# Kernel tuning notes

Hardware: AMD Instinct MI355X
Metric: run time of the kernel (lower is better)

## Reference

```python
import jax, jax.numpy as jnp
import numpy as np


def setup_inputs() -> dict:
    key = jax.random.key(0)
    ks = jax.random.split(key, 11)
    B, n, d_x, d = 8, 2048, 128, 512
    H, hd = 8, 64  # num_heads, head_size = d_v // num_heads
    std_key = d ** -0.5      # d_k ** -0.5 (d_k = 512 after mlp rep)
    std_val = d ** -0.5      # d_v ** -0.5
    return {
        "x1": jax.random.normal(ks[0], (B, n, d_x), jnp.float32),
        "x2": jax.random.normal(ks[1], (B, n, d_x), jnp.float32),
        "r": jax.random.normal(ks[2], (B, n, d), jnp.float32),
        # BatchLinear (shared mlp rep): d_x -> 512 -> 512
        "W1": jax.random.normal(ks[3], (d_x, d), jnp.float32) * (d_x ** -0.5),
        "b1": jnp.zeros((d,), jnp.float32),
        "W2": jax.random.normal(ks[4], (d, d), jnp.float32) * (d ** -0.5),
        "b2": jnp.zeros((d,), jnp.float32),
        # per-head 1x1-conv projections, stacked over heads: [H, out, in]
        "Wq": jax.random.normal(ks[5], (H, hd, d), jnp.float32) * std_key,
        "Wk": jax.random.normal(ks[6], (H, hd, d), jnp.float32) * std_key,
        "Wv": jax.random.normal(ks[7], (H, hd, d), jnp.float32) * std_key,
        "Wo": jax.random.normal(ks[8], (H, d, hd), jnp.float32) * std_val,
    }


def reference(x1, x2, r, W1, b1, W2, b2, Wq, Wk, Wv, Wo):
    # rep == 'mlp': shared BatchLinear applied to x1 (keys) and x2 (queries)
    def mlp(x):  # [B,n,d_x] -> [B,n,512]; relu on all but last layer
        h = jax.nn.relu(jnp.einsum("bnd,de->bne", x, W1) + b1)
        return jnp.einsum("bnd,de->bne", h, W2) + b2

    k = mlp(x1)  # [B,n1,d_k]
    q = mlp(x2)  # [B,n2,d_k]

    # multihead: per-head 1x1 convs == linear projections; batched over heads
    qh = jnp.einsum("bmd,hed->bhme", q, Wq)  # [B,H,m,hd]
    kh = jnp.einsum("bnd,hed->bhne", k, Wk)  # [B,H,n,hd]
    vh = jnp.einsum("bnd,hed->bhne", r, Wv)  # [B,H,n,hd]

    scale = jnp.sqrt(jnp.asarray(qh.shape[-1], qh.dtype))
    scores = jnp.einsum("bhme,bhne->bhmn", qh, kh) / scale
    w = jax.nn.softmax(scores, axis=-1)      # normalise=True
    o = jnp.einsum("bhmn,bhne->bhme", w, vh)  # [B,H,m,hd]

    # per-head output conv (hd -> d_v), summed over heads
    rep = jnp.einsum("bhme,hde->bmd", o, Wo)  # [B,m,d_v]
    return rep
```

## Files before the change

### kernel.cpp

```cpp
#include <hip/hip_runtime.h>
#include <stdint.h>

typedef __attribute__((ext_vector_type(8))) short short8;
typedef __attribute__((ext_vector_type(4))) float f32x4;
typedef __attribute__((ext_vector_type(16))) float f32x16;
typedef __attribute__((ext_vector_type(4))) unsigned u32x4;

#define DEVINL __device__ __forceinline__

DEVINL unsigned short f2bf(float f) {
  unsigned u = __float_as_uint(f);
  u = (u + 0x7FFFu + ((u >> 16) & 1u)) >> 16;
  return (unsigned short)u;
}

DEVINL void gload_lds16(const void* g, void* lds) {
  __builtin_amdgcn_global_load_lds(
      (const __attribute__((address_space(1))) unsigned int*)g,
      (__attribute__((address_space(3))) unsigned int*)lds, 16, 0, 0);
}

DEVINL float fexp2(float x) {
  float r;
  asm("v_exp_f32 %0, %1" : "=v"(r) : "v"(x));
  return r;
}

DEVINL unsigned cvtpk(float lo, float hi) {
  unsigned r;
  asm("v_cvt_pk_bf16_f32 %0, %1, %2" : "=v"(r) : "v"(lo), "v"(hi));
  return r;
}

DEVINL void pl32swap(unsigned& a, unsigned& b) {
  asm("v_permlane32_swap_b32 %0, %1" : "+v"(a), "+v"(b));
}


__global__ void cvt_wquad(const float* __restrict__ W2, const float* __restrict__ Wq,
                          const float* __restrict__ Wk, const float* __restrict__ Wv,
                          unsigned short* __restrict__ W2B, unsigned short* __restrict__ WqB,
                          unsigned short* __restrict__ WkB, unsigned short* __restrict__ WvB) {
  const int a = blockIdx.x >> 8;
  const int i = (blockIdx.x & 255) * 256 + threadIdx.x;
  const float* src = (a == 0) ? W2 : (a == 1) ? Wq : (a == 2) ? Wk : Wv;
  unsigned short* dst = (a == 0) ? W2B : (a == 1) ? WqB : (a == 2) ? WkB : WvB;
  const float scale = (a == 1) ? 0.18033688f : 1.0f;
  float4 v = ((const float4*)src)[i];
  ushort4 o;
  o.x = f2bf(v.x * scale); o.y = f2bf(v.y * scale);
  o.z = f2bf(v.z * scale); o.w = f2bf(v.w * scale);
  ((ushort4*)dst)[i] = o;
}

__global__ void prep_misc(const float* __restrict__ W1, const float* __restrict__ Wo,
                          const float* __restrict__ b2, const float* __restrict__ Wq,
                          const float* __restrict__ Wk,
                          unsigned short* __restrict__ W1T, unsigned short* __restrict__ WoT,
                          float* __restrict__ bqf, float* __restrict__ bkf) {
  const int bid = blockIdx.x, tid = threadIdx.x;
  if (bid < 256) {
    int idx = bid * 256 + tid;
    int n = idx >> 7, k = idx & 127;
    W1T[idx] = f2bf(W1[(size_t)k * 512 + n]);
  } else if (bid < 1280) {
    int idx = (bid - 256) * 256 + tid;
    int d = idx >> 9, j = idx & 511, h = j >> 6, e = j & 63;
    WoT[idx] = f2bf(Wo[(size_t)h * 32768 + (size_t)d * 64 + e]);
  } else {
    int rid = (bid - 1280) * 4 + (tid >> 6);
    int l = tid & 63;
    int e = rid & 511, which = rid >> 9;
    const float* W = which ? Wk : Wq;
    float scale = which ? 1.0f : 0.18033688f;
    float acc = 0.f;
#pragma unroll
    for (int j = 0; j < 8; ++j)
      acc += b2[l * 8 + j] * W[(size_t)e * 512 + l * 8 + j];
    acc *= scale;
#pragma unroll
    for (int off = 1; off < 64; off <<= 1) acc += __shfl_xor(acc, off, 64);
    if (l == 0) (which ? bkf : bqf)[e] = acc;
  }
}

__global__ void cvt_all(const float* __restrict__ x1, const float* __restrict__ x2,
                        const float* __restrict__ r,
                        unsigned short* __restrict__ Xb, unsigned short* __restrict__ Rb) {
  const int bid = blockIdx.x, tid = threadIdx.x;
  const float* src;
  unsigned short* dst;
  int i;
  if (bid < 2048)      { src = x1; dst = Xb;           i = bid * 256 + tid; }
  else if (bid < 4096) { src = x2; dst = Xb + 2097152; i = (bid - 2048) * 256 + tid; }
  else                 { src = r;  dst = Rb;           i = (bid - 4096) * 256 + tid; }
  float4 v = ((const float4*)src)[i];
  ushort4 o;
  o.x = f2bf(v.x); o.y = f2bf(v.y); o.z = f2bf(v.z); o.w = f2bf(v.w);
  ((ushort4*)dst)[i] = o;
}

__global__ __launch_bounds__(256) void v_transpose(const unsigned short* __restrict__ VH,
                                                   unsigned short* __restrict__ VT) {
  const int bh = blockIdx.x, t = blockIdx.y;
  const int b = bh >> 3, h = bh & 7;
  __shared__ __align__(16) unsigned short L[128 * 72];
  const int tid = threadIdx.x;
#pragma unroll
  for (int i = 0; i < 4; ++i) {
    int c = i * 256 + tid, kk = c >> 3, cr = c & 7;
    *(short8*)&L[kk * 72 + cr * 8] =
        *(const short8*)&VH[(size_t)(b * 2048 + t * 128 + kk) * 512 + h * 64 + cr * 8];
  }
  __syncthreads();
#pragma unroll
  for (int i = 0; i < 4; ++i) {
    int c = i * 256 + tid, e = c >> 4, ckn = c & 15;
    short8 v;
#pragma unroll
    for (int j = 0; j < 8; ++j) v[j] = L[(ckn * 8 + j) * 72 + e];
    *(short8*)&VT[((size_t)bh * 64 + e) * 2048 + t * 128 + ckn * 8] = v;
  }
}

template <bool RELU, typename TOut>
__global__ __launch_bounds__(256) void gemm64(
    const unsigned short* A0, const unsigned short* B0, const float* bias0, TOut* C0,
    const unsigned short* A1, const unsigned short* B1, const float* bias1, TOut* C1,
    const unsigned short* A2, const unsigned short* B2, const float* bias2, TOut* C2,
    int M, int N, int K) {
  __shared__ __align__(16) char smem[32768];
  unsigned short* As = (unsigned short*)smem;
  unsigned short* Bs = (unsigned short*)(smem + 16384);

  const int z = blockIdx.z;
  const unsigned short* A = (z == 0) ? A0 : (z == 1) ? A1 : A2;
  const unsigned short* Bt = (z == 0) ? B0 : (z == 1) ? B1 : B2;
  const float* bias = (z == 0) ? bias0 : (z == 1) ? bias1 : bias2;
  TOut* C = (z == 0) ? C0 : (z == 1) ? C1 : C2;

  const int nx = gridDim.x;
  int id = blockIdx.y * nx + blockIdx.x;
  const int nwg = nx * gridDim.y;
  if ((nwg & 7) == 0) id = (id & 7) * (nwg >> 3) + (id >> 3);
  const int n0 = (id % nx) * 128, m0 = (id / nx) * 128;

  const int tid = threadIdx.x, w = tid >> 6, l = tid & 63;
  const int wm = w >> 1, wn = w & 1;
  const int lr = l & 15, lg = l >> 4;

  f32x4 zero4 = {0.f, 0.f, 0.f, 0.f};
  f32x4 acc[4][4];
#pragma unroll
  for (int i = 0; i < 4; ++i)
#pragma unroll
    for (int j = 0; j < 4; ++j) acc[i][j] = zero4;

  for (int k0 = 0; k0 < K; k0 += 64) {
#pragma unroll
    for (int i = 0; i < 4; ++i) {
      const int c = i * 256 + tid;
      const int row = c >> 3, ch = c & 7;
      const int sl = (ch ^ (row & 7)) * 8;
      gload_lds16(A + (size_t)(m0 + row) * K + k0 + sl, (char*)As + c * 16);
      gload_lds16(Bt + (size_t)(n0 + row) * K + k0 + sl, (char*)Bs + c * 16);
    }
    asm volatile("s_waitcnt vmcnt(0)" ::: "memory");
    __syncthreads();

#pragma unroll
    for (int kk = 0; kk < 2; ++kk) {
      short8 af[4], bfr[4];
#pragma unroll
      for (int mi = 0; mi < 4; ++mi) {
        const int row = wm * 64 + mi * 16 + lr;
        af[mi] = *(const short8*)((const char*)As + row * 128 + (((kk * 4 + lg) ^ (row & 7)) * 16));
      }
#pragma unroll
      for (int ni = 0; ni < 4; ++ni) {
        const int row = wn * 64 + ni * 16 + lr;
        bfr[ni] = *(const short8*)((const char*)Bs + row * 128 + (((kk * 4 + lg) ^ (row & 7)) * 16));
      }
#pragma unroll
      for (int mi = 0; mi < 4; ++mi)
#pragma unroll
        for (int ni = 0; ni < 4; ++ni)
          acc[mi][ni] = __builtin_amdgcn_mfma_f32_16x16x32_bf16(af[mi], bfr[ni], acc[mi][ni], 0, 0, 0);
    }
    __syncthreads();
  }

#pragma unroll
  for (int ni = 0; ni < 4; ++ni) {
    const int col = n0 + wn * 64 + ni * 16 + lr;
    const float bv = bias ? bias[col] : 0.f;
#pragma unroll
    for (int mi = 0; mi < 4; ++mi) {
      const int row = m0 + wm * 64 + mi * 16 + lg * 4;
#pragma unroll
      for (int r = 0; r < 4; ++r) {
        float v = acc[mi][ni][r] + bv;
        if (RELU) v = fmaxf(v, 0.f);
        if constexpr (sizeof(TOut) == 2)
          C[(size_t)(row + r) * N + col] = (TOut)f2bf(v);
        else
          C[(size_t)(row + r) * N + col] = v;
      }
    }
  }
}

DEVINL void stage_kv(const unsigned short* Kp, const unsigned short* Vp,
                     char* kb, char* vb, int tid, int k0) {
  const int row = tid >> 3, cs = tid & 7;
  const int sl = (cs ^ (row & 7)) * 8;
  gload_lds16(Kp + (size_t)(k0 + row) * 512 + sl, kb + tid * 16);
  gload_lds16(Vp + (size_t)row * 2048 + k0 + sl, vb + tid * 16);
}

__global__ __launch_bounds__(512) void attn_sw(
    const unsigned short* __restrict__ Q, const unsigned short* __restrict__ Kh,
    const unsigned short* __restrict__ VT, unsigned short* __restrict__ O) {
  const int bh = blockIdx.x, b = bh >> 3, h = bh & 7;
  const int q0 = blockIdx.y * 256;
  const int tid = threadIdx.x, w = tid >> 6, l = tid & 63;
  const int lq = l & 31, hi = l >> 5;
  const size_t baseBH = (size_t)b * 2048 * 512 + (size_t)h * 64;

  __shared__ __align__(16) char smem[49152];
  char* vb0 = smem + 24576;

  const unsigned short* Kp = Kh + baseBH;
  const unsigned short* Vp = VT + (size_t)bh * 64 * 2048;

  short8 qf[4];
  {
    const unsigned short* qp = Q + baseBH + (size_t)(q0 + w * 32 + lq) * 512 + hi * 8;
#pragma unroll
    for (int kc = 0; kc < 4; ++kc) qf[kc] = *(const short8*)(qp + kc * 16);
  }

  f32x16 ot0 = {0,0,0,0,0,0,0,0,0,0,0,0,0,0,0,0};
  f32x16 ot1 = {0,0,0,0,0,0,0,0,0,0,0,0,0,0,0,0};
  float m_run = -1e30f, l_run = 0.f;
  const int xs = (lq & 7);

  stage_kv(Kp, Vp, smem, vb0, tid, 0);
  stage_kv(Kp, Vp, smem + 8192, vb0 + 8192, tid, 64);

  for (int t = 0; t < 32; ++t) {
    if (t < 31) asm volatile("s_waitcnt vmcnt(2)" ::: "memory");
    else        asm volatile("s_waitcnt vmcnt(0)" ::: "memory");
    __syncthreads();
    if (t < 30) {
      const int tn = t + 2, rb = tn - (tn / 3) * 3;
      stage_kv(Kp, Vp, smem + rb * 8192, vb0 + rb * 8192, tid, tn * 64);
    }
    const int cb = t - (t / 3) * 3;
    const char* klc = smem + cb * 8192;
    const char* vtc = vb0 + cb * 8192;

    f32x16 st0 = {0,0,0,0,0,0,0,0,0,0,0,0,0,0,0,0};
    f32x16 st1 = {0,0,0,0,0,0,0,0,0,0,0,0,0,0,0,0};
    __builtin_amdgcn_s_setprio(1);
#pragma unroll
    for (int kc = 0; kc < 4; ++kc) {
      const int sl = ((kc * 2 + hi) ^ xs) * 16;
      short8 kf0 = *(const short8*)(klc + lq * 128 + sl);
      short8 kf1 = *(const short8*)(klc + (32 + lq) * 128 + sl);
      st0 = __builtin_amdgcn_mfma_f32_32x32x16_bf16(kf0, qf[kc], st0, 0, 0, 0);
      st1 = __builtin_amdgcn_mfma_f32_32x32x16_bf16(kf1, qf[kc], st1, 0, 0, 0);
    }
    __builtin_amdgcn_s_setprio(0);

    float t8[8];
#pragma unroll
    for (int r = 0; r < 8; ++r)
      t8[r] = fmaxf(fmaxf(st0[r], st0[r + 8]), fmaxf(st1[r], st1[r + 8]));
    float mt = fmaxf(fmaxf(fmaxf(t8[0], t8[1]), fmaxf(t8[2], t8[3])),
                     fmaxf(fmaxf(t8[4], t8[5]), fmaxf(t8[6], t8[7])));
    mt = fmaxf(mt, __shfl_xor(mt, 32, 64));

    if (__any(mt > m_run + 8.0f)) {
      float mn = fmaxf(m_run, mt);
      float al = fexp2(m_run - mn);
      m_run = mn;
      l_run *= al;
#pragma unroll
      for (int r = 0; r < 16; ++r) { ot0[r] *= al; ot1[r] *= al; }
    }
#pragma unroll
    for (int r = 0; r < 16; ++r) {
      st0[r] = fexp2(st0[r] - m_run);
      st1[r] = fexp2(st1[r] - m_run);
    }
    float s8[8];
#pragma unroll
    for (int r = 0; r < 8; ++r)
      s8[r] = (st0[r] + st0[r + 8]) + (st1[r] + st1[r + 8]);
    float rs = ((s8[0] + s8[1]) + (s8[2] + s8[3])) + ((s8[4] + s8[5]) + (s8[6] + s8[7]));
    rs += __shfl_xor(rs, 32, 64);
    l_run += rs;

    __builtin_amdgcn_s_setprio(1);
#pragma unroll
    for (int kc = 0; kc < 4; ++kc) {
      const int c = kc & 1;
      float p0, p1, p2, p3, p4, p5, p6, p7;
      if (kc < 2) {
        p0 = st0[8*c+0]; p1 = st0[8*c+1]; p2 = st0[8*c+2]; p3 = st0[8*c+3];
        p4 = st0[8*c+4]; p5 = st0[8*c+5]; p6 = st0[8*c+6]; p7 = st0[8*c+7];
      } else {
        p0 = st1[8*c+0]; p1 = st1[8*c+1]; p2 = st1[8*c+2]; p3 = st1[8*c+3];
        p4 = st1[8*c+4]; p5 = st1[8*c+5]; p6 = st1[8*c+6]; p7 = st1[8*c+7];
      }
      unsigned X0 = cvtpk(p0, p1), X1 = cvtpk(p2, p3);
      unsigned Y0 = cvtpk(p4, p5), Y1 = cvtpk(p6, p7);
      pl32swap(X0, Y0);
      pl32swap(X1, Y1);
      u32x4 u = {X0, X1, Y0, Y1};
      short8 pfk = __builtin_bit_cast(short8, u);

      const int sl = ((kc * 2 + hi) ^ xs) * 16;
      short8 v0 = *(const short8*)(vtc + lq * 128 + sl);
      short8 v1 = *(const short8*)(vtc + (32 + lq) * 128 + sl);
      ot0 = __builtin_amdgcn_mfma_f32_32x32x16_bf16(v0, pfk, ot0, 0, 0, 0);
      ot1 = __builtin_amdgcn_mfma_f32_32x32x16_bf16(v1, pfk, ot1, 0, 0, 0);
    }
    __builtin_amdgcn_s_setprio(0);
  }

  __syncthreads();

  unsigned short (*eps)[32][66] = (unsigned short (*)[32][66])smem;
  const float rinv = 1.0f / l_run;
#pragma unroll
  for (int r = 0; r < 16; ++r) {
    const int e = (r & 3) + 8 * (r >> 2) + 4 * hi;
    eps[w][lq][e] = f2bf(ot0[r] * rinv);
    eps[w][lq][e + 32] = f2bf(ot1[r] * rinv);
  }
  asm volatile("s_waitcnt lgkmcnt(0)" ::: "memory");
  __builtin_amdgcn_sched_barrier(0);
#pragma unroll
  for (int i = 0; i < 4; ++i) {
    const int qq = i * 8 + (l >> 3), e0 = (l & 7) * 8;
    short8 v = *(const short8*)&eps[w][qq][e0];
    *(short8*)(O + baseBH + (size_t)(q0 + w * 32 + qq) * 512 + e0) = v;
  }
}


extern "C" void kernel_launch(void* const* d_in, const int* in_sizes, int n_in,
                              void* d_out, int out_size, void* d_ws, size_t ws_size,
                              hipStream_t stream) {
  const float* x1 = (const float*)d_in[0];
  const float* x2 = (const float*)d_in[1];
  const float* r  = (const float*)d_in[2];
  const float* W1 = (const float*)d_in[3];
  const float* b1 = (const float*)d_in[4];
  const float* W2 = (const float*)d_in[5];
  const float* b2 = (const float*)d_in[6];
  const float* Wq = (const float*)d_in[7];
  const float* Wk = (const float*)d_in[8];
  const float* Wv = (const float*)d_in[9];
  const float* Wo = (const float*)d_in[10];

  char* ws = (char*)d_ws;
  size_t off = 0;
  auto alloc = [&](size_t bytes) {
    char* p = ws + off;
    off = (off + bytes + 255) & ~(size_t)255;
    return p;
  };
  unsigned short* W1T = (unsigned short*)alloc(512 * 128 * 2);
  unsigned short* W2B = (unsigned short*)alloc(512 * 512 * 2);
  unsigned short* WqB = (unsigned short*)alloc(512 * 512 * 2);
  unsigned short* WkB = (unsigned short*)alloc(512 * 512 * 2);
  unsigned short* WvB = (unsigned short*)alloc(512 * 512 * 2);
  unsigned short* WoT = (unsigned short*)alloc(512 * 512 * 2);
  unsigned short* Fq  = (unsigned short*)alloc(512 * 512 * 2);
  unsigned short* Fk  = (unsigned short*)alloc(512 * 512 * 2);
  float* bqf = (float*)alloc(512 * 4);
  float* bkf = (float*)alloc(512 * 4);
  unsigned short* Xb  = (unsigned short*)alloc((size_t)32768 * 128 * 2);
  unsigned short* Hb  = (unsigned short*)alloc((size_t)32768 * 512 * 2);
  unsigned short* Rb  = (unsigned short*)alloc((size_t)16384 * 512 * 2);
  unsigned short* QHb = (unsigned short*)alloc((size_t)16384 * 512 * 2);
  unsigned short* KHb = (unsigned short*)alloc((size_t)16384 * 512 * 2);
  unsigned short* VHb = (unsigned short*)alloc((size_t)16384 * 512 * 2);
  unsigned short* VT  = Rb;
  unsigned short* Ob  = QHb;

  cvt_wquad<<<1024, 256, 0, stream>>>(W2, Wq, Wk, Wv, W2B, WqB, WkB, WvB);
  prep_misc<<<1536, 256, 0, stream>>>(W1, Wo, b2, Wq, Wk, W1T, WoT, bqf, bkf);
  gemm64<false, unsigned short><<<dim3(4, 4, 2), 256, 0, stream>>>(
      WqB, W2B, nullptr, Fq,  WkB, W2B, nullptr, Fk,  WkB, W2B, nullptr, Fk,
      512, 512, 512);
  cvt_all<<<12288, 256, 0, stream>>>(x1, x2, r, Xb, Rb);
  gemm64<true, unsigned short><<<dim3(4, 256, 1), 256, 0, stream>>>(
      Xb, W1T, b1, Hb,  Xb, W1T, b1, Hb,  Xb, W1T, b1, Hb,
      32768, 512, 128);
  gemm64<false, unsigned short><<<dim3(4, 128, 3), 256, 0, stream>>>(
      Hb, Fk, bkf, KHb,
      Hb + (size_t)16384 * 512, Fq, bqf, QHb,
      Rb, WvB, nullptr, VHb,
      16384, 512, 512);
  v_transpose<<<dim3(64, 16), 256, 0, stream>>>(VHb, VT);
  attn_sw<<<dim3(64, 8), 512, 0, stream>>>(QHb, KHb, VT, Ob);
  gemm64<false, float><<<dim3(4, 128, 1), 256, 0, stream>>>(
      Ob, WoT, nullptr, (float*)d_out,  Ob, WoT, nullptr, (float*)d_out,
      Ob, WoT, nullptr, (float*)d_out,
      16384, 512, 512);
}
```

Measured before the change: 200.3 us.

## Process two query blocks per wave in attention to reuse K/V fragments

Each wave now handles 64 query rows (two 32-row blocks) instead of 32, so every K and V fragment read from LDS serves two sets of MFMAs, and the grid shrinks from 512 to 256 blocks. K and V fragments are loaded once into registers per tile, and __syncthreads is replaced with a bare s_barrier. The goal is less LDS traffic and fewer global K/V reloads per query, at the cost of more registers per thread and half as many blocks, which may hurt occupancy or load balance on a GPU with many CUs.

```diff
diff --git a/kernel.cpp b/kernel.cpp
--- a/kernel.cpp
+++ b/kernel.cpp
@@ -218,135 +218,165 @@
   gload_lds16(Vp + (size_t)row * 2048 + k0 + sl, vb + tid * 16);
 }
 
-__global__ __launch_bounds__(512) void attn_sw(
+__global__ __launch_bounds__(512, 2) void attn_sw2(
     const unsigned short* __restrict__ Q, const unsigned short* __restrict__ Kh,
     const unsigned short* __restrict__ VT, unsigned short* __restrict__ O) {
   const int bh = blockIdx.x, b = bh >> 3, h = bh & 7;
-  const int q0 = blockIdx.y * 256;
+  const int q0 = blockIdx.y * 512;
   const int tid = threadIdx.x, w = tid >> 6, l = tid & 63;
   const int lq = l & 31, hi = l >> 5;
   const size_t baseBH = (size_t)b * 2048 * 512 + (size_t)h * 64;
 
   __shared__ __align__(16) char smem[49152];
-  char* vb0 = smem + 24576;
 
   const unsigned short* Kp = Kh + baseBH;
   const unsigned short* Vp = VT + (size_t)bh * 64 * 2048;
 
-  short8 qf[4];
-  {
-    const unsigned short* qp = Q + baseBH + (size_t)(q0 + w * 32 + lq) * 512 + hi * 8;
-#pragma unroll
-    for (int kc = 0; kc < 4; ++kc) qf[kc] = *(const short8*)(qp + kc * 16);
-  }
-
-  f32x16 ot0 = {0,0,0,0,0,0,0,0,0,0,0,0,0,0,0,0};
-  f32x16 ot1 = {0,0,0,0,0,0,0,0,0,0,0,0,0,0,0,0};
-  float m_run = -1e30f, l_run = 0.f;
+  short8 qf[2][4];
+#pragma unroll
+  for (int qb = 0; qb < 2; ++qb) {
+    const unsigned short* qp =
+        Q + baseBH + (size_t)(q0 + w * 64 + qb * 32 + lq) * 512 + hi * 8;
+#pragma unroll
+    for (int kc = 0; kc < 4; ++kc) qf[qb][kc] = *(const short8*)(qp + kc * 16);
+  }
+
+  f32x16 ot[2][2];
+#pragma unroll
+  for (int qb = 0; qb < 2; ++qb)
+#pragma unroll
+    for (int eh = 0; eh < 2; ++eh)
+#pragma unroll
+      for (int r = 0; r < 16; ++r) ot[qb][eh][r] = 0.f;
+  float m_run[2] = {-1e30f, -1e30f}, l_run[2] = {0.f, 0.f};
   const int xs = (lq & 7);
 
-  stage_kv(Kp, Vp, smem, vb0, tid, 0);
-  stage_kv(Kp, Vp, smem + 8192, vb0 + 8192, tid, 64);
+  stage_kv(Kp, Vp, smem, smem + 24576, tid, 0);
+  stage_kv(Kp, Vp, smem + 8192, smem + 24576 + 8192, tid, 64);
 
   for (int t = 0; t < 32; ++t) {
     if (t < 31) asm volatile("s_waitcnt vmcnt(2)" ::: "memory");
     else        asm volatile("s_waitcnt vmcnt(0)" ::: "memory");
-    __syncthreads();
+    __builtin_amdgcn_s_barrier();
     if (t < 30) {
       const int tn = t + 2, rb = tn - (tn / 3) * 3;
-      stage_kv(Kp, Vp, smem + rb * 8192, vb0 + rb * 8192, tid, tn * 64);
+      stage_kv(Kp, Vp, smem + rb * 8192, smem + 24576 + rb * 8192, tid, tn * 64);
     }
     const int cb = t - (t / 3) * 3;
     const char* klc = smem + cb * 8192;
-    const char* vtc = vb0 + cb * 8192;
-
-    f32x16 st0 = {0,0,0,0,0,0,0,0,0,0,0,0,0,0,0,0};
-    f32x16 st1 = {0,0,0,0,0,0,0,0,0,0,0,0,0,0,0,0};
+    const char* vtc = smem + 24576 + cb * 8192;
+
+    short8 kf[8];
+#pragma unroll
+    for (int kc = 0; kc < 4; ++kc)
+#pragma unroll
+      for (int kh = 0; kh < 2; ++kh)
+        kf[kc * 2 + kh] =
+            *(const short8*)(klc + (kh * 32 + lq) * 128 + (((kc * 2 + hi) ^ xs) * 16));
+
+    short8 pfk[2][4];
+#pragma unroll
+    for (int qb = 0; qb < 2; ++qb) {
+      f32x16 st0, st1;
+#pragma unroll
+      for (int r = 0; r < 16; ++r) { st0[r] = 0.f; st1[r] = 0.f; }
+      __builtin_amdgcn_s_setprio(1);
+#pragma unroll
+      for (int kc = 0; kc < 4; ++kc) {
+        st0 = __builtin_amdgcn_mfma_f32_32x32x16_bf16(kf[kc * 2 + 0], qf[qb][kc], st0, 0, 0, 0);
+        st1 = __builtin_amdgcn_mfma_f32_32x32x16_bf16(kf[kc * 2 + 1], qf[qb][kc], st1, 0, 0, 0);
+      }
+      __builtin_amdgcn_s_setprio(0);
+
+      float t8[8];
+#pragma unroll
+      for (int r = 0; r < 8; ++r)
+        t8[r] = fmaxf(fmaxf(st0[r], st0[r + 8]), fmaxf(st1[r], st1[r + 8]));
+      float mt = fmaxf(fmaxf(fmaxf(t8[0], t8[1]), fmaxf(t8[2], t8[3])),
+                       fmaxf(fmaxf(t8[4], t8[5]), fmaxf(t8[6], t8[7])));
+      mt = fmaxf(mt, __shfl_xor(mt, 32, 64));
+
+      if (__any(mt > m_run[qb] + 8.0f)) {
+        float mn = fmaxf(m_run[qb], mt);
+        float al = fexp2(m_run[qb] - mn);
+        m_run[qb] = mn;
+        l_run[qb] *= al;
+#pragma unroll
+        for (int r = 0; r < 16; ++r) { ot[qb][0][r] *= al; ot[qb][1][r] *= al; }
+      }
+#pragma unroll
+      for (int r = 0; r < 16; ++r) {
+        st0[r] = fexp2(st0[r] - m_run[qb]);
+        st1[r] = fexp2(st1[r] - m_run[qb]);
+      }
+      float s8[8];
+#pragma unroll
+      for (int r = 0; r < 8; ++r)
+        s8[r] = (st0[r] + st0[r + 8]) + (st1[r] + st1[r + 8]);
+      float rs = ((s8[0] + s8[1]) + (s8[2] + s8[3])) + ((s8[4] + s8[5]) + (s8[6] + s8[7]));
+      rs += __shfl_xor(rs, 32, 64);
+      l_run[qb] += rs;
+
+#pragma unroll
+      for (int kc = 0; kc < 4; ++kc) {
+        const int c = kc & 1;
+        float p0, p1, p2, p3, p4, p5, p6, p7;
+        if (kc < 2) {
+          p0 = st0[8*c+0]; p1 = st0[8*c+1]; p2 = st0[8*c+2]; p3 = st0[8*c+3];
+          p4 = st0[8*c+4]; p5 = st0[8*c+5]; p6 = st0[8*c+6]; p7 = st0[8*c+7];
+        } else {
+          p0 = st1[8*c+0]; p1 = st1[8*c+1]; p2 = st1[8*c+2]; p3 = st1[8*c+3];
+          p4 = st1[8*c+4]; p5 = st1[8*c+5]; p6 = st1[8*c+6]; p7 = st1[8*c+7];
+        }
+        unsigned X0 = cvtpk(p0, p1), X1 = cvtpk(p2, p3);
+        unsigned Y0 = cvtpk(p4, p5), Y1 = cvtpk(p6, p7);
+        pl32swap(X0, Y0);
+        pl32swap(X1, Y1);
+        u32x4 u = {X0, X1, Y0, Y1};
+        pfk[qb][kc] = __builtin_bit_cast(short8, u);
+      }
+    }
+
+    short8 vf[8];
+#pragma unroll
+    for (int kc = 0; kc < 4; ++kc)
+#pragma unroll
+      for (int vh = 0; vh < 2; ++vh)
+        vf[kc * 2 + vh] =
+            *(const short8*)(vtc + (vh * 32 + lq) * 128 + (((kc * 2 + hi) ^ xs) * 16));
+
     __builtin_amdgcn_s_setprio(1);
 #pragma unroll
-    for (int kc = 0; kc < 4; ++kc) {
-      const int sl = ((kc * 2 + hi) ^ xs) * 16;
-      short8 kf0 = *(const short8*)(klc + lq * 128 + sl);
-      short8 kf1 = *(const short8*)(klc + (32 + lq) * 128 + sl);
-      st0 = __builtin_amdgcn_mfma_f32_32x32x16_bf16(kf0, qf[kc], st0, 0, 0, 0);
-      st1 = __builtin_amdgcn_mfma_f32_32x32x16_bf16(kf1, qf[kc], st1, 0, 0, 0);
-    }
+    for (int qb = 0; qb < 2; ++qb)
+#pragma unroll
+      for (int kc = 0; kc < 4; ++kc) {
+        ot[qb][0] = __builtin_amdgcn_mfma_f32_32x32x16_bf16(vf[kc * 2 + 0], pfk[qb][kc], ot[qb][0], 0, 0, 0);
+        ot[qb][1] = __builtin_amdgcn_mfma_f32_32x32x16_bf16(vf[kc * 2 + 1], pfk[qb][kc], ot[qb][1], 0, 0, 0);
+      }
     __builtin_amdgcn_s_setprio(0);
-
-    float t8[8];
-#pragma unroll
-    for (int r = 0; r < 8; ++r)
-      t8[r] = fmaxf(fmaxf(st0[r], st0[r + 8]), fmaxf(st1[r], st1[r + 8]));
-    float mt = fmaxf(fmaxf(fmaxf(t8[0], t8[1]), fmaxf(t8[2], t8[3])),
-                     fmaxf(fmaxf(t8[4], t8[5]), fmaxf(t8[6], t8[7])));
-    mt = fmaxf(mt, __shfl_xor(mt, 32, 64));
-
-    if (__any(mt > m_run + 8.0f)) {
-      float mn = fmaxf(m_run, mt);
-      float al = fexp2(m_run - mn);
-      m_run = mn;
-      l_run *= al;
-#pragma unroll
-      for (int r = 0; r < 16; ++r) { ot0[r] *= al; ot1[r] *= al; }
-    }
+  }
+
+  __syncthreads();
+
+  unsigned short (*eps)[32][68] = (unsigned short (*)[32][68])smem;
+#pragma unroll
+  for (int qb = 0; qb < 2; ++qb) {
+    const float rinv = 1.0f / l_run[qb];
 #pragma unroll
     for (int r = 0; r < 16; ++r) {
-      st0[r] = fexp2(st0[r] - m_run);
-      st1[r] = fexp2(st1[r] - m_run);
-    }
-    float s8[8];
-#pragma unroll
-    for (int r = 0; r < 8; ++r)
-      s8[r] = (st0[r] + st0[r + 8]) + (st1[r] + st1[r + 8]);
-    float rs = ((s8[0] + s8[1]) + (s8[2] + s8[3])) + ((s8[4] + s8[5]) + (s8[6] + s8[7]));
-    rs += __shfl_xor(rs, 32, 64);
-    l_run += rs;
-
-    __builtin_amdgcn_s_setprio(1);
-#pragma unroll
-    for (int kc = 0; kc < 4; ++kc) {
-      const int c = kc & 1;
-      float p0, p1, p2, p3, p4, p5, p6, p7;
-      if (kc < 2) {
-        p0 = st0[8*c+0]; p1 = st0[8*c+1]; p2 = st0[8*c+2]; p3 = st0[8*c+3];
-        p4 = st0[8*c+4]; p5 = st0[8*c+5]; p6 = st0[8*c+6]; p7 = st0[8*c+7];
-      } else {
-        p0 = st1[8*c+0]; p1 = st1[8*c+1]; p2 = st1[8*c+2]; p3 = st1[8*c+3];
-        p4 = st1[8*c+4]; p5 = st1[8*c+5]; p6 = st1[8*c+6]; p7 = st1[8*c+7];
-      }
-      unsigned X0 = cvtpk(p0, p1), X1 = cvtpk(p2, p3);
-      unsigned Y0 = cvtpk(p4, p5), Y1 = cvtpk(p6, p7);
-      pl32swap(X0, Y0);
-      pl32swap(X1, Y1);
-      u32x4 u = {X0, X1, Y0, Y1};
-      short8 pfk = __builtin_bit_cast(short8, u);
-
-      const int sl = ((kc * 2 + hi) ^ xs) * 16;
-      short8 v0 = *(const short8*)(vtc + lq * 128 + sl);
-      short8 v1 = *(const short8*)(vtc + (32 + lq) * 128 + sl);
-      ot0 = __builtin_amdgcn_mfma_f32_32x32x16_bf16(v0, pfk, ot0, 0, 0, 0);
-      ot1 = __builtin_amdgcn_mfma_f32_32x32x16_bf16(v1, pfk, ot1, 0, 0, 0);
-    }
-    __builtin_amdgcn_s_setprio(0);
-  }
-
-  __syncthreads();
-
-  unsigned short (*eps)[32][66] = (unsigned short (*)[32][66])smem;
-  const float rinv = 1.0f / l_run;
-#pragma unroll
-  for (int r = 0; r < 16; ++r) {
-    const int e = (r & 3) + 8 * (r >> 2) + 4 * hi;
-    eps[w][lq][e] = f2bf(ot0[r] * rinv);
-    eps[w][lq][e + 32] = f2bf(ot1[r] * rinv);
-  }
-  asm volatile("s_waitcnt lgkmcnt(0)" ::: "memory");
-  __builtin_amdgcn_sched_barrier(0);
-#pragma unroll
-  for (int i = 0; i < 4; ++i) {
-    const int qq = i * 8 + (l >> 3), e0 = (l & 7) * 8;
-    short8 v = *(const short8*)&eps[w][qq][e0];
-    *(short8*)(O + baseBH + (size_t)(q0 + w * 32 + qq) * 512 + e0) = v;
+      const int e = (r & 3) + 8 * (r >> 2) + 4 * hi;
+      eps[w][lq][e] = f2bf(ot[qb][0][r] * rinv);
+      eps[w][lq][e + 32] = f2bf(ot[qb][1][r] * rinv);
+    }
+    asm volatile("s_waitcnt lgkmcnt(0)" ::: "memory");
+    __builtin_amdgcn_sched_barrier(0);
+#pragma unroll
+    for (int i = 0; i < 4; ++i) {
+      const int qq = i * 8 + (l >> 3), e0 = (l & 7) * 8;
+      short8 v = *(const short8*)&eps[w][qq][e0];
+      *(short8*)(O + baseBH + (size_t)(q0 + w * 64 + qb * 32 + qq) * 512 + e0) = v;
+    }
+    __builtin_amdgcn_sched_barrier(0);
   }
 }
 
@@ -407,7 +437,7 @@
       Rb, WvB, nullptr, VHb,
       16384, 512, 512);
   v_transpose<<<dim3(64, 16), 256, 0, stream>>>(VHb, VT);
-  attn_sw<<<dim3(64, 8), 512, 0, stream>>>(QHb, KHb, VT, Ob);
+  attn_sw2<<<dim3(64, 4), 512, 0, stream>>>(QHb, KHb, VT, Ob);
   gemm64<false, float><<<dim3(4, 128, 1), 256, 0, stream>>>(
       Ob, WoT, nullptr, (float*)d_out,  Ob, WoT, nullptr, (float*)d_out,
       Ob, WoT, nullptr, (float*)d_out,
```

Measured after the change: 208.3 us. 1.04x slower.

## Compute V projection transposed directly, drop transpose kernel, overlap GEMM staging

Applied to the files above, without the earlier changes.

The V projection is now computed as WvB x Rb^T, so the GEMM writes V already transposed into a [512,16384] buffer that the attention kernel reads with a new stride. This removes the separate v_transpose kernel and its global round trip. The GEMM kernel also issues the next tile's global-to-LDS load after reading fragments into registers, so the load overlaps the MFMAs. A single 1D grid with per-z N and tile counts replaces the 2D grid. The change costs an extra buffer allocation and longer register lifetimes for the fragments.

```diff
diff --git a/kernel.cpp b/kernel.cpp
--- a/kernel.cpp
+++ b/kernel.cpp
@@ -100,35 +100,12 @@
   ((ushort4*)dst)[i] = o;
 }
 
-__global__ __launch_bounds__(256) void v_transpose(const unsigned short* __restrict__ VH,
-                                                   unsigned short* __restrict__ VT) {
-  const int bh = blockIdx.x, t = blockIdx.y;
-  const int b = bh >> 3, h = bh & 7;
-  __shared__ __align__(16) unsigned short L[128 * 72];
-  const int tid = threadIdx.x;
-#pragma unroll
-  for (int i = 0; i < 4; ++i) {
-    int c = i * 256 + tid, kk = c >> 3, cr = c & 7;
-    *(short8*)&L[kk * 72 + cr * 8] =
-        *(const short8*)&VH[(size_t)(b * 2048 + t * 128 + kk) * 512 + h * 64 + cr * 8];
-  }
-  __syncthreads();
-#pragma unroll
-  for (int i = 0; i < 4; ++i) {
-    int c = i * 256 + tid, e = c >> 4, ckn = c & 15;
-    short8 v;
-#pragma unroll
-    for (int j = 0; j < 8; ++j) v[j] = L[(ckn * 8 + j) * 72 + e];
-    *(short8*)&VT[((size_t)bh * 64 + e) * 2048 + t * 128 + ckn * 8] = v;
-  }
-}
-
 template <bool RELU, typename TOut>
 __global__ __launch_bounds__(256) void gemm64(
-    const unsigned short* A0, const unsigned short* B0, const float* bias0, TOut* C0,
-    const unsigned short* A1, const unsigned short* B1, const float* bias1, TOut* C1,
-    const unsigned short* A2, const unsigned short* B2, const float* bias2, TOut* C2,
-    int M, int N, int K) {
+    const unsigned short* A0, const unsigned short* B0, const float* bias0, TOut* C0, int N0, int nx0,
+    const unsigned short* A1, const unsigned short* B1, const float* bias1, TOut* C1, int N1, int nx1,
+    const unsigned short* A2, const unsigned short* B2, const float* bias2, TOut* C2, int N2, int nx2,
+    int K) {
   __shared__ __align__(16) char smem[32768];
   unsigned short* As = (unsigned short*)smem;
   unsigned short* Bs = (unsigned short*)(smem + 16384);
@@ -138,16 +115,18 @@
   const unsigned short* Bt = (z == 0) ? B0 : (z == 1) ? B1 : B2;
   const float* bias = (z == 0) ? bias0 : (z == 1) ? bias1 : bias2;
   TOut* C = (z == 0) ? C0 : (z == 1) ? C1 : C2;
-
-  const int nx = gridDim.x;
-  int id = blockIdx.y * nx + blockIdx.x;
-  const int nwg = nx * gridDim.y;
+  const int N = (z == 0) ? N0 : (z == 1) ? N1 : N2;
+  const int nx = (z == 0) ? nx0 : (z == 1) ? nx1 : nx2;
+
+  int id = blockIdx.x;
+  const int nwg = gridDim.x;
   if ((nwg & 7) == 0) id = (id & 7) * (nwg >> 3) + (id >> 3);
   const int n0 = (id % nx) * 128, m0 = (id / nx) * 128;
 
   const int tid = threadIdx.x, w = tid >> 6, l = tid & 63;
   const int wm = w >> 1, wn = w & 1;
   const int lr = l & 15, lg = l >> 4;
+  const int nt = K >> 6;
 
   f32x4 zero4 = {0.f, 0.f, 0.f, 0.f};
   f32x4 acc[4][4];
@@ -156,38 +135,46 @@
 #pragma unroll
     for (int j = 0; j < 4; ++j) acc[i][j] = zero4;
 
-  for (int k0 = 0; k0 < K; k0 += 64) {
+  auto STAGE = [&](int t) {
 #pragma unroll
     for (int i = 0; i < 4; ++i) {
       const int c = i * 256 + tid;
       const int row = c >> 3, ch = c & 7;
       const int sl = (ch ^ (row & 7)) * 8;
-      gload_lds16(A + (size_t)(m0 + row) * K + k0 + sl, (char*)As + c * 16);
-      gload_lds16(Bt + (size_t)(n0 + row) * K + k0 + sl, (char*)Bs + c * 16);
-    }
+      gload_lds16(A + (size_t)(m0 + row) * K + t * 64 + sl, (char*)As + c * 16);
+      gload_lds16(Bt + (size_t)(n0 + row) * K + t * 64 + sl, (char*)Bs + c * 16);
+    }
+  };
+
+  STAGE(0);
+  for (int t = 0; t < nt; ++t) {
     asm volatile("s_waitcnt vmcnt(0)" ::: "memory");
-    __syncthreads();
-
+    __builtin_amdgcn_s_barrier();
+    short8 af[2][4], bfr[2][4];
 #pragma unroll
     for (int kk = 0; kk < 2; ++kk) {
-      short8 af[4], bfr[4];
 #pragma unroll
       for (int mi = 0; mi < 4; ++mi) {
         const int row = wm * 64 + mi * 16 + lr;
-        af[mi] = *(const short8*)((const char*)As + row * 128 + (((kk * 4 + lg) ^ (row & 7)) * 16));
+        af[kk][mi] = *(const short8*)((const char*)As + row * 128 + (((kk * 4 + lg) ^ (row & 7)) * 16));
       }
 #pragma unroll
       for (int ni = 0; ni < 4; ++ni) {
         const int row = wn * 64 + ni * 16 + lr;
-        bfr[ni] = *(const short8*)((const char*)Bs + row * 128 + (((kk * 4 + lg) ^ (row & 7)) * 16));
+        bfr[kk][ni] = *(const short8*)((const char*)Bs + row * 128 + (((kk * 4 + lg) ^ (row & 7)) * 16));
       }
+    }
+    asm volatile("s_waitcnt lgkmcnt(0)" ::: "memory");
+    __builtin_amdgcn_s_barrier();
+    if (t + 1 < nt) STAGE(t + 1);
+    __builtin_amdgcn_sched_barrier(0);
+#pragma unroll
+    for (int kk = 0; kk < 2; ++kk)
 #pragma unroll
       for (int mi = 0; mi < 4; ++mi)
 #pragma unroll
         for (int ni = 0; ni < 4; ++ni)
-          acc[mi][ni] = __builtin_amdgcn_mfma_f32_16x16x32_bf16(af[mi], bfr[ni], acc[mi][ni], 0, 0, 0);
-    }
-    __syncthreads();
+          acc[mi][ni] = __builtin_amdgcn_mfma_f32_16x16x32_bf16(af[kk][mi], bfr[kk][ni], acc[mi][ni], 0, 0, 0);
   }
 
 #pragma unroll
@@ -215,12 +202,12 @@
   const int row = tid >> 3, cs = tid & 7;
   const int sl = (cs ^ (row & 7)) * 8;
   gload_lds16(Kp + (size_t)(k0 + row) * 512 + sl, kb + tid * 16);
-  gload_lds16(Vp + (size_t)row * 2048 + k0 + sl, vb + tid * 16);
+  gload_lds16(Vp + (size_t)row * 16384 + k0 + sl, vb + tid * 16);
 }
 
 __global__ __launch_bounds__(512) void attn_sw(
     const unsigned short* __restrict__ Q, const unsigned short* __restrict__ Kh,
-    const unsigned short* __restrict__ VT, unsigned short* __restrict__ O) {
+    const unsigned short* __restrict__ VT2, unsigned short* __restrict__ O) {
   const int bh = blockIdx.x, b = bh >> 3, h = bh & 7;
   const int q0 = blockIdx.y * 256;
   const int tid = threadIdx.x, w = tid >> 6, l = tid & 63;
@@ -231,7 +218,7 @@
   char* vb0 = smem + 24576;
 
   const unsigned short* Kp = Kh + baseBH;
-  const unsigned short* Vp = VT + (size_t)bh * 64 * 2048;
+  const unsigned short* Vp = VT2 + (size_t)(h * 64) * 16384 + (size_t)b * 2048;
 
   short8 qf[4];
   {
@@ -251,7 +238,7 @@
   for (int t = 0; t < 32; ++t) {
     if (t < 31) asm volatile("s_waitcnt vmcnt(2)" ::: "memory");
     else        asm volatile("s_waitcnt vmcnt(0)" ::: "memory");
-    __syncthreads();
+    __builtin_amdgcn_s_barrier();
     if (t < 30) {
       const int tn = t + 2, rb = tn - (tn / 3) * 3;
       stage_kv(Kp, Vp, smem + rb * 8192, vb0 + rb * 8192, tid, tn * 64);
@@ -388,28 +375,31 @@
   unsigned short* Rb  = (unsigned short*)alloc((size_t)16384 * 512 * 2);
   unsigned short* QHb = (unsigned short*)alloc((size_t)16384 * 512 * 2);
   unsigned short* KHb = (unsigned short*)alloc((size_t)16384 * 512 * 2);
-  unsigned short* VHb = (unsigned short*)alloc((size_t)16384 * 512 * 2);
-  unsigned short* VT  = Rb;
+  unsigned short* VT2 = (unsigned short*)alloc((size_t)512 * 16384 * 2);
   unsigned short* Ob  = QHb;
 
   cvt_wquad<<<1024, 256, 0, stream>>>(W2, Wq, Wk, Wv, W2B, WqB, WkB, WvB);
   prep_misc<<<1536, 256, 0, stream>>>(W1, Wo, b2, Wq, Wk, W1T, WoT, bqf, bkf);
-  gemm64<false, unsigned short><<<dim3(4, 4, 2), 256, 0, stream>>>(
-      WqB, W2B, nullptr, Fq,  WkB, W2B, nullptr, Fk,  WkB, W2B, nullptr, Fk,
-      512, 512, 512);
+  gemm64<false, unsigned short><<<dim3(16, 1, 2), 256, 0, stream>>>(
+      WqB, W2B, nullptr, Fq, 512, 4,
+      WkB, W2B, nullptr, Fk, 512, 4,
+      WkB, W2B, nullptr, Fk, 512, 4,
+      512);
   cvt_all<<<12288, 256, 0, stream>>>(x1, x2, r, Xb, Rb);
-  gemm64<true, unsigned short><<<dim3(4, 256, 1), 256, 0, stream>>>(
-      Xb, W1T, b1, Hb,  Xb, W1T, b1, Hb,  Xb, W1T, b1, Hb,
-      32768, 512, 128);
-  gemm64<false, unsigned short><<<dim3(4, 128, 3), 256, 0, stream>>>(
-      Hb, Fk, bkf, KHb,
-      Hb + (size_t)16384 * 512, Fq, bqf, QHb,
-      Rb, WvB, nullptr, VHb,
-      16384, 512, 512);
-  v_transpose<<<dim3(64, 16), 256, 0, stream>>>(VHb, VT);
-  attn_sw<<<dim3(64, 8), 512, 0, stream>>>(QHb, KHb, VT, Ob);
-  gemm64<false, float><<<dim3(4, 128, 1), 256, 0, stream>>>(
-      Ob, WoT, nullptr, (float*)d_out,  Ob, WoT, nullptr, (float*)d_out,
-      Ob, WoT, nullptr, (float*)d_out,
-      16384, 512, 512);
-}
+  gemm64<true, unsigned short><<<dim3(1024, 1, 1), 256, 0, stream>>>(
+      Xb, W1T, b1, Hb, 512, 4,
+      Xb, W1T, b1, Hb, 512, 4,
+      Xb, W1T, b1, Hb, 512, 4,
+      128);
+  gemm64<false, unsigned short><<<dim3(512, 1, 3), 256, 0, stream>>>(
+      Hb, Fk, bkf, KHb, 512, 4,
+      Hb + (size_t)16384 * 512, Fq, bqf, QHb, 512, 4,
+      WvB, Rb, nullptr, VT2, 16384, 128,
+      512);
+  attn_sw<<<dim3(64, 8), 512, 0, stream>>>(QHb, KHb, VT2, Ob);
+  gemm64<false, float><<<dim3(512, 1, 1), 256, 0, stream>>>(
+      Ob, WoT, nullptr, (float*)d_out, 512, 4,
+      Ob, WoT, nullptr, (float*)d_out, 512, 4,
+      Ob, WoT, nullptr, (float*)d_out, 512, 4,
+      512);
+}
```

Result: faster. 186.8 us (-6.8%).
